# Kernel tuning notes

Hardware: AMD Instinct MI355X
Metric: run time of the kernel (lower is better)

The kernel has to match this reference:

```python
import jax, jax.numpy as jnp
import numpy as np

D_MODEL = 512
D_STATE = 128
D_CONV = 4
EXPAND = 2
HEADDIM = 64
D_INNER = EXPAND * D_MODEL            # 1024
NHEADS = D_INNER // HEADDIM           # 16
CONV_DIM = D_INNER + 2 * D_STATE      # 1280
D_IN_PROJ = 2 * D_INNER + 2 * D_STATE + NHEADS  # 2320
EPS = 1e-5


def _mamba2(u, in_w, conv_w, conv_b, A_log, dt_bias, Dp, norm_w, out_w):
    # u: [b, l, d_model]  -- Mamba2 forward (ngroups=1), SSD in exact quadratic form
    b, l, _ = u.shape
    zxbcdt = u @ in_w.T                                   # [b,l,2320]
    z = zxbcdt[..., :D_INNER]
    xBC = zxbcdt[..., D_INNER:D_INNER + CONV_DIM]
    dt = zxbcdt[..., D_INNER + CONV_DIM:]                 # [b,l,nheads]
    # causal depthwise conv1d (kernel 4) + silu
    xp = jnp.pad(xBC, ((0, 0), (D_CONV - 1, 0), (0, 0)))
    conv = sum(xp[:, k:k + l, :] * conv_w[:, k] for k in range(D_CONV))
    xBC = jax.nn.silu(conv + conv_b)
    x = xBC[..., :D_INNER].reshape(b, l, NHEADS, HEADDIM)
    Bm = xBC[..., D_INNER:D_INNER + D_STATE]              # [b,l,d_state]
    Cm = xBC[..., D_INNER + D_STATE:]                     # [b,l,d_state]
    dt = jax.nn.softplus(dt + dt_bias)                    # [b,l,nheads]
    dtA = dt * (-jnp.exp(A_log))                          # [b,l,nheads], negative
    # SSD quadratic (semiseparable) form: L[t,s] = exp(sum_{r=s+1..t} dtA_r), causal
    cs = jnp.cumsum(dtA, axis=1)                          # [b,l,nh]
    seg = cs[:, :, None, :] - cs[:, None, :, :]           # [b,t,s,nh]
    mask = jnp.tril(jnp.ones((l, l), bool))
    L = jnp.exp(jnp.where(mask[None, :, :, None], seg, -jnp.inf))
    G = jnp.einsum('btd,bsd->bts', Cm, Bm)                # C_t . B_s
    dtx = dt[..., None] * x                               # [b,l,nh,hd]
    y = jnp.einsum('btsn,bsnp->btnp', G[..., None] * L, dtx)
    y = (y + x * Dp[:, None]).reshape(b, l, D_INNER)      # D skip
    # gated RMSNorm (norm_before_gate=False): rmsnorm(y * silu(z)) * weight
    y = y * jax.nn.silu(z)
    y = y * jax.lax.rsqrt(jnp.mean(jnp.square(y), -1, keepdims=True) + EPS) * norm_w
    return y @ out_w.T


def _forward(x, h_in_w, h_conv_w, h_conv_b, h_A_log, h_dt_bias, h_D, h_norm_w, h_out_w,
             v_in_w, v_conv_w, v_conv_b, v_A_log, v_dt_bias, v_D, v_norm_w, v_out_w,
             fc_w, fc_b):
    B, H, W, C = x.shape
    hp = (h_in_w, h_conv_w, h_conv_b, h_A_log, h_dt_bias, h_D, h_norm_w, h_out_w)
    vp = (v_in_w, v_conv_w, v_conv_b, v_A_log, v_dt_bias, v_D, v_norm_w, v_out_w)
    # horizontal: scan along W for each (B*H) row
    xh = x.reshape(-1, W, C)
    h1 = _mamba2(xh, *hp)
    # NOTE: original code flips dim 0 (batch), reproduced faithfully
    h2 = jnp.flip(_mamba2(jnp.flip(xh, 0), *hp), 0)
    h = jnp.concatenate([h1, h2], -1).reshape(B, H, W, -1)
    # vertical: scan along H for each (B*W) column
    xv = jnp.transpose(x, (0, 2, 1, 3)).reshape(-1, H, C)
    v1 = _mamba2(xv, *vp)
    v2 = jnp.flip(_mamba2(jnp.flip(xv, 0), *vp), 0)
    v = jnp.transpose(jnp.concatenate([v1, v2], -1).reshape(B, W, H, -1), (0, 2, 1, 3))
    out = jnp.concatenate([v, h], -1) @ fc_w.T + fc_b     # [B,H,W,C]
    return out


def setup_inputs() -> dict:
    key = jax.random.key(0)
    ks = jax.random.split(key, 8)
    B, H, W, C = 2, 64, 64, D_MODEL
    x = jax.random.normal(ks[0], (B, H, W, C), jnp.float32)

    def mk(k):
        kk = jax.random.split(k, 5)
        return {
            'in_w': 0.02 * jax.random.normal(kk[0], (D_IN_PROJ, D_MODEL), jnp.float32),
            'conv_w': 0.1 * jax.random.normal(kk[1], (CONV_DIM, D_CONV), jnp.float32),
            'conv_b': jnp.zeros((CONV_DIM,), jnp.float32),
            'A_log': jnp.log(jax.random.uniform(kk[2], (NHEADS,), jnp.float32, 1.0, 16.0)),
            'dt_bias': jnp.log(jnp.expm1(jax.random.uniform(kk[3], (NHEADS,), jnp.float32, 1e-3, 0.1))),
            'D': jnp.ones((NHEADS,), jnp.float32),
            'norm_w': jnp.ones((D_INNER,), jnp.float32),
            'out_w': 0.02 * jax.random.normal(kk[4], (D_MODEL, D_INNER), jnp.float32),
        }

    hp, vp = mk(ks[1]), mk(ks[2])
    inp = {'x': x}
    inp.update({f'h_{n}': v for n, v in hp.items()})
    inp.update({f'v_{n}': v for n, v in vp.items()})
    inp['fc_w'] = 0.02 * jax.random.normal(ks[3], (D_MODEL, 4 * D_MODEL), jnp.float32)
    inp['fc_b'] = jnp.zeros((D_MODEL,), jnp.float32)
    return inp


def reference(x, h_in_w, h_conv_w, h_conv_b, h_A_log, h_dt_bias, h_D, h_norm_w, h_out_w,
              v_in_w, v_conv_w, v_conv_b, v_A_log, v_dt_bias, v_D, v_norm_w, v_out_w,
              fc_w, fc_b):
    return _forward(x, h_in_w, h_conv_w, h_conv_b, h_A_log, h_dt_bias, h_D, h_norm_w, h_out_w,
                    v_in_w, v_conv_w, v_conv_b, v_A_log, v_dt_bias, v_D, v_norm_w, v_out_w,
                    fc_w, fc_b)
```

## Files before the change

### kernel.cpp

```cpp
#include <hip/hip_runtime.h>

#define NROWS 8192
#define NZX   2304
#define BCS   136
#define XMS   72

#define PB0 4096
#define PB1 (PB0 + 2048)
#define PB2 (PB1 + 2304)
#define PB3 (PB2 + 256)
#define PB4 (PB3 + 512)

typedef __attribute__((ext_vector_type(8))) short bf16x8;
typedef __attribute__((ext_vector_type(4))) float f32x4;

__device__ __forceinline__ float bf2f(unsigned short u) {
    union { unsigned int i; float f; } v; v.i = ((unsigned int)u) << 16; return v.f;
}
__device__ __forceinline__ unsigned short f2bf(float f) {
    union { float f; unsigned int i; } v; v.f = f;
    return (unsigned short)((v.i + 0x8000u) >> 16);
}

__device__ __forceinline__ void async_lds16(const unsigned short* g, unsigned short* l) {
    __builtin_amdgcn_global_load_lds(
        (const __attribute__((address_space(1))) unsigned int*)g,
        (__attribute__((address_space(3))) unsigned int*)l, 16, 0, 0);
}

__global__ __launch_bounds__(256) void prep_kernel(
    const float* __restrict__ x, const float* __restrict__ fcw,
    const float* __restrict__ iw0, const float* __restrict__ iw1,
    const float* __restrict__ ow0, const float* __restrict__ ow1,
    const float* __restrict__ db0, const float* __restrict__ db1,
    const float* __restrict__ al0, const float* __restrict__ al1,
    unsigned short* __restrict__ xbf, unsigned short* __restrict__ wf,
    unsigned short* __restrict__ wbA, unsigned short* __restrict__ wbOT0,
    unsigned short* __restrict__ wbOT1, float* __restrict__ dtbb,
    float* __restrict__ csbb)
{
    __shared__ char sm[37888] __attribute__((aligned(16)));
    const int blk = blockIdx.x, tid = threadIdx.x;
    if (blk < PB0) {
        int i = blk * 256 + tid;
        float4 v = *(const float4*)(x + (size_t)i * 4);
        ushort4 o;
        o.x = f2bf(v.x); o.y = f2bf(v.y); o.z = f2bf(v.z); o.w = f2bf(v.w);
        *(ushort4*)(xbf + (size_t)i * 4) = o;
    } else if (blk < PB1) {
        int idx = (blk - PB0) * 256 + tid;
        int o = idx >> 10, c = idx & 1023;
        int half = c >> 9, cc = c & 511;
        float v = fcw[(size_t)o * 2048 + half * 1024 + cc] +
                  fcw[(size_t)o * 2048 + half * 1024 + 512 + cc];
        wf[idx] = f2bf(v);
    } else if (blk < PB2) {
        int local = blk - PB1;
        int dir = local / 1152;
        int i = (local % 1152) * 256 + tid;
        const float* s = dir ? iw1 : iw0;
        float4 v = *(const float4*)(s + (size_t)i * 4);
        ushort4 o;
        o.x = f2bf(v.x); o.y = f2bf(v.y); o.z = f2bf(v.z); o.w = f2bf(v.w);
        *(ushort4*)(wbA + (size_t)dir * (2304 * 512) + (size_t)i * 4) = o;
    } else if (blk < PB3) {
        float (*T)[65] = (float(*)[65])sm;
        int local = blk - PB2;
        int z = local >> 7, rem = local & 127;
        const float* s = z ? ow1 : ow0;
        unsigned short* d = z ? wbOT1 : wbOT0;
        const int bo = (rem >> 4) * 64, bc = (rem & 15) * 64;
#pragma unroll
        for (int i = 0; i < 16; ++i) {
            int slot = tid + i * 256;
            int r = slot >> 6, c = slot & 63;
            T[r][c] = s[(size_t)(bo + r) * 1024 + bc + c];
        }
        __syncthreads();
#pragma unroll
        for (int i = 0; i < 16; ++i) {
            int slot = tid + i * 256;
            int cr = slot >> 6, oc = slot & 63;
            d[(size_t)(bc + cr) * 512 + bo + oc] = f2bf(T[oc][cr]);
        }
    } else {
        float (*wsm)[512] = (float(*)[512])sm;
        float (*xs)[68]   = (float(*)[68])(sm + 16384);
        float (*dta)[64]  = (float(*)[64])(sm + 16384 + 17408);
        float (*dtt)[64]  = (float(*)[64])(sm + 16384 + 17408 + 2048);
        int local = blk - PB3;
        const int dir = local >> 8, bxl = local & 255;
        const float* in_w = dir ? iw1 : iw0;
        const float* dt_bias = dir ? db1 : db0;
        const float* A_log = dir ? al1 : al0;
        float* dtb = dtbb + (size_t)dir * 131072;
        float* csb = csbb + (size_t)dir * 131072;
        const int seq = bxl >> 1, hq = bxl & 1;
#pragma unroll
        for (int i = 0; i < 4; ++i) {
            int slot = tid + i * 256;
            int h = slot >> 7, c = (slot & 127) * 4;
            *(float4*)&wsm[h][c] = *(const float4*)(in_w + (size_t)(2304 + hq * 8 + h) * 512 + c);
        }
        const int t = tid & 63, hg = tid >> 6;
        float acc[2] = {0.f, 0.f};
        for (int c0 = 0; c0 < 512; c0 += 64) {
            __syncthreads();
#pragma unroll
            for (int i = 0; i < 4; ++i) {
                int slot = tid + i * 256;
                int r = slot >> 4, cc = (slot & 15) * 4;
                size_t row = (dir == 0) ? (size_t)seq * 64 + r
                                        : (size_t)(seq >> 6) * 4096 + (size_t)r * 64 + (seq & 63);
                *(float4*)&xs[r][cc] = *(const float4*)(x + row * 512 + c0 + cc);
            }
            __syncthreads();
#pragma unroll
            for (int cc = 0; cc < 64; cc += 4) {
                float4 u4 = *(const float4*)&xs[t][cc];
                const float* w0 = &wsm[hg * 2][c0 + cc];
                const float* w1 = &wsm[hg * 2 + 1][c0 + cc];
                acc[0] += u4.x * w0[0] + u4.y * w0[1] + u4.z * w0[2] + u4.w * w0[3];
                acc[1] += u4.x * w1[0] + u4.y * w1[1] + u4.z * w1[2] + u4.w * w1[3];
            }
        }
#pragma unroll
        for (int hh = 0; hh < 2; ++hh) {
            int hl = hg * 2 + hh;
            int h = hq * 8 + hl;
            float v = acc[hh] + dt_bias[h];
            float dtv = (v > 20.f) ? v : log1pf(__expf(v));
            dtt[hl][t] = dtv;
            dta[hl][t] = dtv * -__expf(A_log[h]);
        }
        __syncthreads();
        if (tid < 8) {
            float run = 0.f;
            int ob = (seq * 16 + hq * 8 + tid) * 64;
            for (int tt = 0; tt < 64; ++tt) {
                run += dta[tid][tt];
                dtb[ob + tt] = dtt[tid][tt];
                csb[ob + tt] = run;
            }
        }
    }
}

struct GemmEpi { unsigned short* C; int ldc; int colsub; int conv; };

template<int QA, int QB>
__device__ __forceinline__ void phase_mma(
    const unsigned short* AS, const unsigned short* BS, int cb,
    const int (&aoff)[4], const int (&boff)[2], const int (&kcx)[2],
    f32x4 (&acc)[8][4])
{
    const unsigned short* Ab = AS + cb * 16384 + QA * 8192;
    const unsigned short* Bb = BS + cb * 16384 + QB * 8192;
    bf16x8 av[2][4], bv[2][2];
#pragma unroll
    for (int kh = 0; kh < 2; ++kh) {
#pragma unroll
        for (int f = 0; f < 4; ++f) av[kh][f] = *(const bf16x8*)(Ab + aoff[f] + kcx[kh]);
#pragma unroll
        for (int g = 0; g < 2; ++g) bv[kh][g] = *(const bf16x8*)(Bb + boff[g] + kcx[kh]);
    }
    __builtin_amdgcn_s_setprio(1);
#pragma unroll
    for (int f = 0; f < 4; ++f)
#pragma unroll
        for (int g = 0; g < 2; ++g)
#pragma unroll
            for (int kh = 0; kh < 2; ++kh)
                acc[QA * 4 + f][QB * 2 + g] = __builtin_amdgcn_mfma_f32_16x16x32_bf16(
                    av[kh][f], bv[kh][g], acc[QA * 4 + f][QB * 2 + g], 0, 0, 0);
    __builtin_amdgcn_s_setprio(0);
}

__global__ __launch_bounds__(512) void gemm_big(
    const unsigned short* __restrict__ xbf, const unsigned short* __restrict__ wbA,
    unsigned short* __restrict__ zx, const unsigned short* __restrict__ wf,
    const unsigned short* __restrict__ wbOT0, const unsigned short* __restrict__ wbOT1,
    unsigned short* __restrict__ wcomb, const float* __restrict__ cw0,
    const float* __restrict__ cw1, const float* __restrict__ cb0,
    const float* __restrict__ cb1, unsigned short* __restrict__ xbc)
{
    __shared__ unsigned short SMEM[65536] __attribute__((aligned(16)));
    unsigned short* AS = SMEM;
    unsigned short* BS = SMEM + 32768;
    const int bx = blockIdx.x, z = blockIdx.z;
    const unsigned short *A, *B;
    int lda, perm, mB, nB;
    GemmEpi epi;
    if (bx < 288) {
        int xcd = bx & 7, l = bx >> 3;
        int cid = xcd * 36 + l;
        int mt = cid / 9, nt = cid - mt * 9;
        mB = mt * 256; nB = nt * 256;
        A = xbf; lda = 512; perm = z;
        B = wbA + (size_t)z * (2304 * 512);
        if (nB >= 1024) { epi.C = xbc + (size_t)z * NROWS * 1280; epi.ldc = 1280; epi.colsub = 1024; epi.conv = 1; }
        else            { epi.C = zx + (size_t)z * NROWS * NZX;  epi.ldc = NZX;  epi.colsub = 0;    epi.conv = 0; }
    } else {
        int t2 = bx - 288;
        mB = (t2 >> 2) * 256; nB = (t2 & 3) * 256;
        A = z ? wf : wf + 512; lda = 1024; perm = 0;
        B = z ? wbOT1 : wbOT0;
        epi.C = z ? wcomb : wcomb + 1024; epi.ldc = 2048; epi.colsub = 0; epi.conv = 0;
    }
    const int tid = threadIdx.x, wave = tid >> 6, lane = tid & 63;
    const int wr = wave >> 2, wc = wave & 3;
    const int lr = lane & 15, lq = lane >> 4;
    const unsigned short* gA[2][2];
    const unsigned short* gB[2][2];
    int ldsSlot[2];
#pragma unroll
    for (int i = 0; i < 2; ++i) {
        int s = tid + i * 512;
        int r = s >> 3, p = s & 7, q = p ^ (r & 7);
        ldsSlot[i] = s * 8;
#pragma unroll
        for (int h = 0; h < 2; ++h) {
            int ar = mB + h * 128 + r;
            if (perm) ar = (ar & ~4095) | ((ar & 63) << 6) | ((ar >> 6) & 63);
            gA[i][h] = A + (size_t)ar * lda + q * 8;
            gB[i][h] = B + (size_t)(nB + h * 128 + r) * 512 + q * 8;
        }
    }
    int aoff[4], boff[2], kcx[2];
#pragma unroll
    for (int f = 0; f < 4; ++f) aoff[f] = (wr * 64 + f * 16 + lr) * 64;
#pragma unroll
    for (int g = 0; g < 2; ++g) boff[g] = (wc * 32 + g * 16 + lr) * 64;
#pragma unroll
    for (int kh = 0; kh < 2; ++kh) kcx[kh] = ((kh * 4 + lq) ^ (lr & 7)) * 8;
    f32x4 acc[8][4];
#pragma unroll
    for (int m = 0; m < 8; ++m)
#pragma unroll
        for (int n = 0; n < 4; ++n) acc[m][n] = (f32x4){0.f, 0.f, 0.f, 0.f};

#define STAGE_A(H, K0, CB) { _Pragma("unroll") \
    for (int i = 0; i < 2; ++i) async_lds16(gA[i][H] + (K0), AS + (CB) * 16384 + (H) * 8192 + ldsSlot[i]); }
#define STAGE_B(H, K0, CB) { _Pragma("unroll") \
    for (int i = 0; i < 2; ++i) async_lds16(gB[i][H] + (K0), BS + (CB) * 16384 + (H) * 8192 + ldsSlot[i]); }

    STAGE_A(0, 0, 0); STAGE_B(0, 0, 0); STAGE_A(1, 0, 0); STAGE_B(1, 0, 0);
#pragma unroll 1
    for (int t = 0; t < 7; ++t) {
        const int cb = t & 1, nb2 = cb ^ 1, k1 = (t + 1) * 64;
        asm volatile("s_waitcnt vmcnt(4)" ::: "memory");
        asm volatile("s_barrier" ::: "memory");
        STAGE_A(0, k1, nb2);
        phase_mma<0, 0>(AS, BS, cb, aoff, boff, kcx, acc);
        asm volatile("s_waitcnt vmcnt(4)" ::: "memory");
        asm volatile("s_barrier" ::: "memory");
        STAGE_B(0, k1, nb2);
        phase_mma<1, 0>(AS, BS, cb, aoff, boff, kcx, acc);
        asm volatile("s_waitcnt vmcnt(4)" ::: "memory");
        asm volatile("s_barrier" ::: "memory");
        STAGE_A(1, k1, nb2);
        phase_mma<0, 1>(AS, BS, cb, aoff, boff, kcx, acc);
        STAGE_B(1, k1, nb2);
        phase_mma<1, 1>(AS, BS, cb, aoff, boff, kcx, acc);
    }
    asm volatile("s_waitcnt vmcnt(0)" ::: "memory");
    asm volatile("s_barrier" ::: "memory");
    phase_mma<0, 0>(AS, BS, 1, aoff, boff, kcx, acc);
    phase_mma<1, 0>(AS, BS, 1, aoff, boff, kcx, acc);
    phase_mma<0, 1>(AS, BS, 1, aoff, boff, kcx, acc);
    phase_mma<1, 1>(AS, BS, 1, aoff, boff, kcx, acc);

    unsigned short* WR = BS + wave * 1024;
    const int rsl = (lane + 48) & 63;
    if (epi.conv) {
        float4 wv[4]; float bb[4];
#pragma unroll
        for (int c4 = 0; c4 < 4; ++c4) {
            int col = nB - 1024 + (c4 >> 1) * 128 + wc * 32 + (c4 & 1) * 16 + lr;
            const float* cwp = z ? cw1 : cw0;
            const float* cbp = z ? cb1 : cb0;
            wv[c4] = *(const float4*)(cwp + (size_t)col * 4);
            bb[c4] = cbp[col];
        }
#pragma unroll
        for (int h = 0; h < 2; ++h) {
            float pr1[4], pr2[4], pr3[4];
#pragma unroll
            for (int c4 = 0; c4 < 4; ++c4) { pr1[c4] = 0.f; pr2[c4] = 0.f; pr3[c4] = 0.f; }
#pragma unroll
            for (int f = 0; f < 4; ++f) {
#pragma unroll
                for (int c4 = 0; c4 < 4; ++c4) {
                    float vq[4];
#pragma unroll
                    for (int r = 0; r < 4; ++r) vq[r] = acc[h * 4 + f][c4][r];
                    float rc1 = __shfl(vq[1], rsl);
                    float rc2 = __shfl(vq[2], rsl);
                    float rc3 = __shfl(vq[3], rsl);
                    float u1 = lq ? rc3 : pr3[c4];
                    float u2 = lq ? rc2 : pr2[c4];
                    float u3 = lq ? rc1 : pr1[c4];
                    pr1[c4] = rc1; pr2[c4] = rc2; pr3[c4] = rc3;
                    float y4[4];
                    y4[0] = bb[c4] + wv[c4].w*vq[0] + wv[c4].z*u1    + wv[c4].y*u2    + wv[c4].x*u3;
                    y4[1] = bb[c4] + wv[c4].w*vq[1] + wv[c4].z*vq[0] + wv[c4].y*u1    + wv[c4].x*u2;
                    y4[2] = bb[c4] + wv[c4].w*vq[2] + wv[c4].z*vq[1] + wv[c4].y*vq[0] + wv[c4].x*u1;
                    y4[3] = bb[c4] + wv[c4].w*vq[3] + wv[c4].z*vq[2] + wv[c4].y*vq[1] + wv[c4].x*vq[0];
#pragma unroll
                    for (int r = 0; r < 4; ++r) {
                        float a = y4[r];
                        float s = a / (1.f + __expf(-a));
                        int r16 = lq * 4 + r;
                        int cn = c4 * 16 + lr;
                        int gp = ((cn >> 3) + (r16 >> 1)) & 7;
                        WR[r16 * 64 + gp * 8 + (cn & 7)] = f2bf(s);
                    }
                }
#pragma unroll
                for (int j = 0; j < 2; ++j) {
                    int r16 = j * 8 + (lane >> 3);
                    int gr = lane & 7;
                    int gp = (gr + (r16 >> 1)) & 7;
                    uint4 v = *(const uint4*)(WR + r16 * 64 + gp * 8);
                    int row = mB + h * 128 + wr * 64 + f * 16 + r16;
                    int col = nB - epi.colsub + (gr >> 2) * 128 + wc * 32 + ((gr >> 1) & 1) * 16 + (gr & 1) * 8;
                    *(uint4*)(epi.C + (size_t)row * epi.ldc + col) = v;
                }
            }
        }
    } else {
#pragma unroll
        for (int h = 0; h < 2; ++h)
#pragma unroll
            for (int f = 0; f < 4; ++f) {
#pragma unroll
                for (int c4 = 0; c4 < 4; ++c4)
#pragma unroll
                    for (int r = 0; r < 4; ++r) {
                        int r16 = lq * 4 + r;
                        int cn = c4 * 16 + lr;
                        int gp = ((cn >> 3) + (r16 >> 1)) & 7;
                        WR[r16 * 64 + gp * 8 + (cn & 7)] = f2bf(acc[h * 4 + f][c4][r]);
                    }
#pragma unroll
                for (int j = 0; j < 2; ++j) {
                    int r16 = j * 8 + (lane >> 3);
                    int gr = lane & 7;
                    int gp = (gr + (r16 >> 1)) & 7;
                    uint4 v = *(const uint4*)(WR + r16 * 64 + gp * 8);
                    int row = mB + h * 128 + wr * 64 + f * 16 + r16;
                    int col = nB + (gr >> 2) * 128 + wc * 32 + ((gr >> 1) & 1) * 16 + (gr & 1) * 8;
                    *(uint4*)(epi.C + (size_t)row * epi.ldc + col) = v;
                }
            }
    }
#undef STAGE_A
#undef STAGE_B
}

__global__ __launch_bounds__(256) void gemm_final2048(
    const unsigned short* __restrict__ YV, const unsigned short* __restrict__ YH,
    const unsigned short* __restrict__ W, const float* __restrict__ bias,
    float* __restrict__ C)
{
    __shared__ unsigned short As[128 * 64];
    __shared__ unsigned short Bs[64 * 64];
    const int tid = threadIdx.x, wave = tid >> 6, lane = tid & 63;
    const int did = blockIdx.y * 64 + blockIdx.x;
    const int mB = (did >> 3) * 128, nB = (did & 7) * 64;
    const int lr = lane & 15, lq = lane >> 4;
    int aq[4], agr[4], apr[4];
    unsigned short* lA[4];
    const unsigned short* BgP[2];
    unsigned short* lB[2];
#pragma unroll
    for (int i = 0; i < 4; ++i) {
        int s = tid + i * 256;
        int r = s >> 3, p = s & 7;
        aq[i] = (p ^ (r & 7)) * 8;
        int gr = mB + r;
        agr[i] = gr;
        apr[i] = (gr & ~4095) | ((gr & 63) << 6) | ((gr >> 6) & 63);
        lA[i] = As + s * 8;
    }
#pragma unroll
    for (int i = 0; i < 2; ++i) {
        int s = tid + i * 256;
        int r = s >> 3, p = s & 7;
        int q = p ^ (r & 7);
        BgP[i] = W + (size_t)(nB + r) * 2048 + q * 8;
        lB[i] = Bs + s * 8;
    }
    const int aswz = lr & 7;
    int arb[2], brb[4];
#pragma unroll
    for (int i = 0; i < 2; ++i) arb[i] = (wave * 32 + i * 16 + lr) * 64;
#pragma unroll
    for (int i = 0; i < 4; ++i) brb[i] = (i * 16 + lr) * 64;
    f32x4 zero4 = {0.f,0.f,0.f,0.f};
    f32x4 acc[2][4] = {{zero4,zero4,zero4,zero4},{zero4,zero4,zero4,zero4}};
    for (int k0 = 0; k0 < 2048; k0 += 64) {
#pragma unroll
        for (int i = 0; i < 4; ++i) {
            int kk = k0 + aq[i];
            const unsigned short* g = (kk < 1024)
                ? YV + (size_t)apr[i] * 1024 + kk
                : YH + (size_t)agr[i] * 1024 + (kk - 1024);
            async_lds16(g, lA[i]);
        }
#pragma unroll
        for (int i = 0; i < 2; ++i) async_lds16(BgP[i] + k0, lB[i]);
        __syncthreads();
#pragma unroll
        for (int kh = 0; kh < 2; ++kh) {
            const int ksw = ((kh * 4 + lq) ^ aswz) * 8;
            bf16x8 a[2], b[4];
#pragma unroll
            for (int i = 0; i < 2; ++i) a[i] = *(const bf16x8*)(As + arb[i] + ksw);
#pragma unroll
            for (int i = 0; i < 4; ++i) b[i] = *(const bf16x8*)(Bs + brb[i] + ksw);
#pragma unroll
            for (int mi = 0; mi < 2; ++mi)
#pragma unroll
                for (int ni = 0; ni < 4; ++ni)
                    acc[mi][ni] = __builtin_amdgcn_mfma_f32_16x16x32_bf16(
                        a[mi], b[ni], acc[mi][ni], 0, 0, 0);
        }
        __syncthreads();
    }
    const int rbase = lq * 4;
#pragma unroll
    for (int mi = 0; mi < 2; ++mi)
#pragma unroll
        for (int ni = 0; ni < 4; ++ni) {
            int col = nB + ni * 16 + lr;
            float bb = bias[col];
#pragma unroll
            for (int r = 0; r < 4; ++r) {
                int row = mB + wave * 32 + mi * 16 + rbase + r;
                C[(size_t)row * 512 + col] = acc[mi][ni][r] + bb;
            }
        }
}

__global__ __launch_bounds__(256) void gmat_kernel(
    const unsigned short* __restrict__ xbcb, float* __restrict__ Gbuf)
{
    __shared__ unsigned short Bs[64 * BCS];
    __shared__ unsigned short Cs[64 * BCS];
    const int dir = blockIdx.y, seq = blockIdx.x;
    const unsigned short* base = xbcb + (size_t)dir * NROWS * 1280
                                      + (size_t)seq * 64 * 1280;
    const int tid = threadIdx.x;
    const int lane = tid & 63, wave = tid >> 6;
#pragma unroll
    for (int i = 0; i < 4; ++i) {
        int e = (tid + i * 256) * 8;
        int r = e >> 7, c = e & 127;
        *(uint4*)(Bs + r * BCS + c) = *(const uint4*)(base + (size_t)r * 1280 + 1024 + c);
        *(uint4*)(Cs + r * BCS + c) = *(const uint4*)(base + (size_t)r * 1280 + 1152 + c);
    }
    __syncthreads();
    const int lr = lane & 15, lq = lane >> 4;
    f32x4 zero4 = {0.f,0.f,0.f,0.f};
    f32x4 acc[4] = {zero4, zero4, zero4, zero4};
#pragma unroll
    for (int kt = 0; kt < 4; ++kt) {
        bf16x8 a = *(const bf16x8*)(Cs + (wave * 16 + lr) * BCS + kt * 32 + lq * 8);
#pragma unroll
        for (int ni = 0; ni < 4; ++ni) {
            bf16x8 b = *(const bf16x8*)(Bs + (ni * 16 + lr) * BCS + kt * 32 + lq * 8);
            acc[ni] = __builtin_amdgcn_mfma_f32_16x16x32_bf16(a, b, acc[ni], 0, 0, 0);
        }
    }
    float* G = Gbuf + ((size_t)dir * 128 + seq) * 4096;
#pragma unroll
    for (int ni = 0; ni < 4; ++ni) {
        int s = ni * 16 + lr;
#pragma unroll
        for (int r = 0; r < 4; ++r) {
            int t = wave * 16 + lq * 4 + r;
            G[t * 64 + s] = acc[ni][r];
        }
    }
}

__global__ __launch_bounds__(256) void scan_kernel(
    const unsigned short* __restrict__ xbcb, const float* __restrict__ Gbuf,
    const float* __restrict__ dtbb, const float* __restrict__ csbb,
    const float* __restrict__ Dv0, const float* __restrict__ Dv1,
    unsigned short* __restrict__ yh, unsigned short* __restrict__ yv)
{
    __shared__ unsigned short XsT[64 * XMS];
    __shared__ unsigned short Ms[64 * XMS];
    __shared__ float dts[64], css[64];
    const int dir = blockIdx.y;
    const unsigned short* xbc = xbcb + (size_t)dir * NROWS * 1280;
    const float* dtb = dtbb + (size_t)dir * 131072;
    const float* csb = csbb + (size_t)dir * 131072;
    const float* Dv = dir ? Dv1 : Dv0;
    unsigned short* y = dir ? yv : yh;
    const int tid = threadIdx.x;
    const int lane = tid & 63, wave = tid >> 6;
    const int seq = blockIdx.x >> 4, h = blockIdx.x & 15;
    if (tid < 64) {
        dts[tid] = dtb[(seq * 16 + h) * 64 + tid];
        css[tid] = csb[(seq * 16 + h) * 64 + tid];
    }
    const unsigned short* base = xbc + (size_t)seq * 64 * 1280;
#pragma unroll
    for (int i = 0; i < 2; ++i) {
        int e = (tid + i * 256) * 8;
        int t = e >> 6, p0 = e & 63;
        uint4 xval = *(const uint4*)(base + (size_t)t * 1280 + h * 64 + p0);
        const unsigned short* xs = (const unsigned short*)&xval;
#pragma unroll
        for (int j = 0; j < 8; ++j) {
            int jl = (j + lane) & 7;
            XsT[(p0 + jl) * XMS + t] = xs[jl];
        }
    }
    const int lr = lane & 15, lq = lane >> 4;
    const float* G = Gbuf + ((size_t)dir * 128 + seq) * 4096;
    f32x4 acc[4];
#pragma unroll
    for (int ni = 0; ni < 4; ++ni) {
        int s = ni * 16 + lr;
#pragma unroll
        for (int r = 0; r < 4; ++r) {
            int t = wave * 16 + lq * 4 + r;
            acc[ni][r] = G[t * 64 + s];
        }
    }
    __syncthreads();
    float css_t[4];
#pragma unroll
    for (int r = 0; r < 4; ++r) css_t[r] = css[wave * 16 + lq * 4 + r];
#pragma unroll
    for (int ni = 0; ni < 4; ++ni) {
        int s = ni * 16 + lr;
        float cs_s = css[s], dt_s = dts[s];
#pragma unroll
        for (int r = 0; r < 4; ++r) {
            int t = wave * 16 + lq * 4 + r;
            float e = __expf(fminf(css_t[r] - cs_s, 0.f));
            float m = (s <= t) ? acc[ni][r] * e * dt_s : 0.f;
            Ms[t * XMS + s] = f2bf(m);
        }
    }
    __syncthreads();
    f32x4 zero4 = {0.f,0.f,0.f,0.f};
    f32x4 yacc[4] = {zero4, zero4, zero4, zero4};
#pragma unroll
    for (int kt = 0; kt < 2; ++kt) {
        bf16x8 a = *(const bf16x8*)(Ms + (wave * 16 + lr) * XMS + kt * 32 + lq * 8);
#pragma unroll
        for (int ni = 0; ni < 4; ++ni) {
            bf16x8 b = *(const bf16x8*)(XsT + (ni * 16 + lr) * XMS + kt * 32 + lq * 8);
            yacc[ni] = __builtin_amdgcn_mfma_f32_16x16x32_bf16(a, b, yacc[ni], 0, 0, 0);
        }
    }
    const float Dh = Dv[h];
#pragma unroll
    for (int ni = 0; ni < 4; ++ni) {
        int p = ni * 16 + lr;
#pragma unroll
        for (int r = 0; r < 4; ++r) {
            int t = wave * 16 + lq * 4 + r;
            float v = yacc[ni][r] + Dh * bf2f(XsT[p * XMS + t]);
            Ms[t * XMS + p] = f2bf(v);
        }
    }
    __syncthreads();
    unsigned short* yout = y + (size_t)seq * 64 * 1024 + h * 64;
#pragma unroll
    for (int i = 0; i < 2; ++i) {
        int slot = tid + i * 256;
        int t = slot >> 3, pc = (slot & 7) * 8;
        uint4 v = *(const uint4*)(Ms + t * XMS + pc);
        *(uint4*)(yout + (size_t)t * 1024 + pc) = v;
    }
}

__global__ __launch_bounds__(128) void gate_norm(
    const unsigned short* __restrict__ zxb, unsigned short* __restrict__ yh,
    unsigned short* __restrict__ yv, const float* __restrict__ nw0,
    const float* __restrict__ nw1)
{
    const int dir = blockIdx.y;
    const unsigned short* zx = zxb + (size_t)dir * NROWS * NZX;
    unsigned short* y = dir ? yv : yh;
    const float* nw = dir ? nw1 : nw0;
    const int row = blockIdx.x, tid = threadIdx.x;
    uint4 yv4 = *(const uint4*)(y + (size_t)row * 1024 + tid * 8);
    uint4 zv4 = *(const uint4*)(zx + (size_t)row * NZX + tid * 8);
    const unsigned short* ys = (const unsigned short*)&yv4;
    const unsigned short* zs = (const unsigned short*)&zv4;
    float g[8]; float ss = 0.f;
#pragma unroll
    for (int j = 0; j < 8; ++j) {
        float zv = bf2f(zs[j]);
        float gv = bf2f(ys[j]) * (zv / (1.f + __expf(-zv)));
        g[j] = gv; ss += gv * gv;
    }
#pragma unroll
    for (int off = 32; off > 0; off >>= 1) ss += __shfl_xor(ss, off, 64);
    __shared__ float red[2];
    if ((tid & 63) == 0) red[tid >> 6] = ss;
    __syncthreads();
    ss = red[0] + red[1];
    const float scale = rsqrtf(ss * (1.f / 1024.f) + 1e-5f);
    unsigned short out8[8] __attribute__((aligned(16)));
#pragma unroll
    for (int j = 0; j < 8; ++j) out8[j] = f2bf(g[j] * scale * nw[tid * 8 + j]);
    *(uint4*)(y + (size_t)row * 1024 + tid * 8) = *(const uint4*)out8;
}

extern "C" void kernel_launch(void* const* d_in, const int* in_sizes, int n_in,
                              void* d_out, int out_size, void* d_ws, size_t ws_size,
                              hipStream_t stream)
{
    (void)in_sizes; (void)n_in; (void)out_size; (void)ws_size;
    const float* x   = (const float*)d_in[0];
    const float* fcw = (const float*)d_in[17];
    const float* fcb = (const float*)d_in[18];
    const float* iw0 = (const float*)d_in[1];  const float* iw1 = (const float*)d_in[9];
    const float* cw0 = (const float*)d_in[2];  const float* cw1 = (const float*)d_in[10];
    const float* cb0 = (const float*)d_in[3];  const float* cb1 = (const float*)d_in[11];
    const float* al0 = (const float*)d_in[4];  const float* al1 = (const float*)d_in[12];
    const float* db0 = (const float*)d_in[5];  const float* db1 = (const float*)d_in[13];
    const float* Dv0 = (const float*)d_in[6];  const float* Dv1 = (const float*)d_in[14];
    const float* nw0 = (const float*)d_in[7];  const float* nw1 = (const float*)d_in[15];
    const float* ow0 = (const float*)d_in[8];  const float* ow1 = (const float*)d_in[16];

    char* ws = (char*)d_ws;
    size_t off = 0;
    auto alloc = [&](size_t bytes) {
        void* p = ws + off; off += (bytes + 255) & ~(size_t)255; return p;
    };
    unsigned short* xbf   = (unsigned short*)alloc((size_t)NROWS * 512 * 2);
    unsigned short* wbA   = (unsigned short*)alloc((size_t)2 * 2304 * 512 * 2);
    unsigned short* wbOT0 = (unsigned short*)alloc((size_t)1024 * 512 * 2);
    unsigned short* wbOT1 = (unsigned short*)alloc((size_t)1024 * 512 * 2);
    unsigned short* wf    = (unsigned short*)alloc((size_t)512 * 1024 * 2);
    unsigned short* wcomb = (unsigned short*)alloc((size_t)512 * 2048 * 2);
    unsigned short* zx    = (unsigned short*)alloc((size_t)2 * NROWS * NZX * 2);
    unsigned short* xbc   = (unsigned short*)alloc((size_t)2 * NROWS * 1280 * 2);
    float* Gbuf           = (float*)alloc((size_t)2 * 128 * 4096 * 4);
    float* dtb            = (float*)alloc((size_t)2 * 2048 * 64 * 4);
    float* csb            = (float*)alloc((size_t)2 * 2048 * 64 * 4);
    unsigned short* ybh   = (unsigned short*)alloc((size_t)NROWS * 1024 * 2);
    unsigned short* ybv   = (unsigned short*)alloc((size_t)NROWS * 1024 * 2);

    prep_kernel<<<PB4, 256, 0, stream>>>(x, fcw, iw0, iw1, ow0, ow1, db0, db1,
                                         al0, al1, xbf, wf, wbA, wbOT0, wbOT1,
                                         dtb, csb);
    gemm_big<<<dim3(296, 1, 2), 512, 0, stream>>>(xbf, wbA, zx, wf,
                                                  wbOT0, wbOT1, wcomb,
                                                  cw0, cw1, cb0, cb1, xbc);
    gmat_kernel<<<dim3(128, 2), 256, 0, stream>>>(xbc, Gbuf);
    scan_kernel<<<dim3(2048, 2), 256, 0, stream>>>(xbc, Gbuf, dtb, csb,
                                                   Dv0, Dv1, ybh, ybv);
    gate_norm<<<dim3(NROWS, 2), 128, 0, stream>>>(zx, ybh, ybv, nw0, nw1);
    gemm_final2048<<<dim3(64, 8), 256, 0, stream>>>(ybv, ybh, wcomb, fcb, (float*)d_out);
}
```

Baseline: 282.7 us.

## Restructure GEMM main loop into two half-phases reusing B fragments

Replaces the four quarter-phase MMA steps per k-tile with two half-phases. The first half loads all B fragments once and keeps them in registers for the second half, which cuts LDS reads of B and halves the barriers per iteration. The async staging order and vmcnt waits are reordered to match the new phase boundaries. The trade-off is higher register pressure from holding B fragments and coarser-grained overlap between loads and MFMA work.

```diff
diff --git a/kernel.cpp b/kernel.cpp
--- a/kernel.cpp
+++ b/kernel.cpp
@@ -148,31 +148,38 @@
 
 struct GemmEpi { unsigned short* C; int ldc; int colsub; int conv; };
 
-template<int QA, int QB>
-__device__ __forceinline__ void phase_mma(
-    const unsigned short* AS, const unsigned short* BS, int cb,
+template<int QA, bool LOADB>
+__device__ __forceinline__ void mma_half(
+    const unsigned short* Ab, const unsigned short* Bb,
     const int (&aoff)[4], const int (&boff)[2], const int (&kcx)[2],
-    f32x4 (&acc)[8][4])
-{
-    const unsigned short* Ab = AS + cb * 16384 + QA * 8192;
-    const unsigned short* Bb = BS + cb * 16384 + QB * 8192;
-    bf16x8 av[2][4], bv[2][2];
-#pragma unroll
-    for (int kh = 0; kh < 2; ++kh) {
-#pragma unroll
-        for (int f = 0; f < 4; ++f) av[kh][f] = *(const bf16x8*)(Ab + aoff[f] + kcx[kh]);
-#pragma unroll
-        for (int g = 0; g < 2; ++g) bv[kh][g] = *(const bf16x8*)(Bb + boff[g] + kcx[kh]);
+    bf16x8 (&bv)[2][2][2], f32x4 (&acc)[8][4])
+{
+    bf16x8 av[4][2];
+#pragma unroll
+    for (int f = 0; f < 4; ++f)
+#pragma unroll
+        for (int kh = 0; kh < 2; ++kh)
+            av[f][kh] = *(const bf16x8*)(Ab + QA * 8192 + aoff[f] + kcx[kh]);
+    if (LOADB) {
+#pragma unroll
+        for (int h = 0; h < 2; ++h)
+#pragma unroll
+            for (int g = 0; g < 2; ++g)
+#pragma unroll
+                for (int kh = 0; kh < 2; ++kh)
+                    bv[h][g][kh] = *(const bf16x8*)(Bb + h * 8192 + boff[g] + kcx[kh]);
     }
     __builtin_amdgcn_s_setprio(1);
 #pragma unroll
     for (int f = 0; f < 4; ++f)
 #pragma unroll
-        for (int g = 0; g < 2; ++g)
-#pragma unroll
-            for (int kh = 0; kh < 2; ++kh)
-                acc[QA * 4 + f][QB * 2 + g] = __builtin_amdgcn_mfma_f32_16x16x32_bf16(
-                    av[kh][f], bv[kh][g], acc[QA * 4 + f][QB * 2 + g], 0, 0, 0);
+        for (int h = 0; h < 2; ++h)
+#pragma unroll
+            for (int g = 0; g < 2; ++g)
+#pragma unroll
+                for (int kh = 0; kh < 2; ++kh)
+                    acc[QA * 4 + f][h * 2 + g] = __builtin_amdgcn_mfma_f32_16x16x32_bf16(
+                        av[f][kh], bv[h][g][kh], acc[QA * 4 + f][h * 2 + g], 0, 0, 0);
     __builtin_amdgcn_s_setprio(0);
 }
 
@@ -244,31 +251,33 @@
 #define STAGE_B(H, K0, CB) { _Pragma("unroll") \
     for (int i = 0; i < 2; ++i) async_lds16(gB[i][H] + (K0), BS + (CB) * 16384 + (H) * 8192 + ldsSlot[i]); }
 
-    STAGE_A(0, 0, 0); STAGE_B(0, 0, 0); STAGE_A(1, 0, 0); STAGE_B(1, 0, 0);
+    STAGE_A(0, 0, 0); STAGE_B(0, 0, 0); STAGE_B(1, 0, 0); STAGE_A(1, 0, 0);
 #pragma unroll 1
     for (int t = 0; t < 7; ++t) {
         const int cb = t & 1, nb2 = cb ^ 1, k1 = (t + 1) * 64;
+        const unsigned short* Ab = AS + cb * 16384;
+        const unsigned short* Bb = BS + cb * 16384;
+        bf16x8 bv[2][2][2];
+        asm volatile("s_waitcnt vmcnt(2)" ::: "memory");
+        asm volatile("s_barrier" ::: "memory");
+        STAGE_A(0, k1, nb2); STAGE_B(0, k1, nb2);
+        mma_half<0, true>(Ab, Bb, aoff, boff, kcx, bv, acc);
         asm volatile("s_waitcnt vmcnt(4)" ::: "memory");
         asm volatile("s_barrier" ::: "memory");
-        STAGE_A(0, k1, nb2);
-        phase_mma<0, 0>(AS, BS, cb, aoff, boff, kcx, acc);
-        asm volatile("s_waitcnt vmcnt(4)" ::: "memory");
+        STAGE_B(1, k1, nb2); STAGE_A(1, k1, nb2);
+        mma_half<1, false>(Ab, Bb, aoff, boff, kcx, bv, acc);
+    }
+    {
+        const unsigned short* Ab = AS + 16384;
+        const unsigned short* Bb = BS + 16384;
+        bf16x8 bv[2][2][2];
+        asm volatile("s_waitcnt vmcnt(2)" ::: "memory");
         asm volatile("s_barrier" ::: "memory");
-        STAGE_B(0, k1, nb2);
-        phase_mma<1, 0>(AS, BS, cb, aoff, boff, kcx, acc);
-        asm volatile("s_waitcnt vmcnt(4)" ::: "memory");
+        mma_half<0, true>(Ab, Bb, aoff, boff, kcx, bv, acc);
+        asm volatile("s_waitcnt vmcnt(0)" ::: "memory");
         asm volatile("s_barrier" ::: "memory");
-        STAGE_A(1, k1, nb2);
-        phase_mma<0, 1>(AS, BS, cb, aoff, boff, kcx, acc);
-        STAGE_B(1, k1, nb2);
-        phase_mma<1, 1>(AS, BS, cb, aoff, boff, kcx, acc);
-    }
-    asm volatile("s_waitcnt vmcnt(0)" ::: "memory");
-    asm volatile("s_barrier" ::: "memory");
-    phase_mma<0, 0>(AS, BS, 1, aoff, boff, kcx, acc);
-    phase_mma<1, 0>(AS, BS, 1, aoff, boff, kcx, acc);
-    phase_mma<0, 1>(AS, BS, 1, aoff, boff, kcx, acc);
-    phase_mma<1, 1>(AS, BS, 1, aoff, boff, kcx, acc);
+        mma_half<1, false>(Ab, Bb, aoff, boff, kcx, bv, acc);
+    }
 
     unsigned short* WR = BS + wave * 1024;
     const int rsl = (lane + 48) & 63;
```

Result: no change. 283.0 us (+0.1%).
